# Optimization experiments

Measured on AMD Instinct MI355X. Metric: run time of the kernel, lower is better.

The kernel has to match this reference:

```python
import jax, jax.numpy as jnp
from jax import lax
import numpy as np

# Static module configuration (matches init_kwargs, idx=0)
B, T, H, W, C = 2, 8, 64, 64, 128
T_SP, H_SP, W_SP = 2, 64, 4          # idx=0 -> H_sp=resolution, W_sp=split_size
NUM_HEADS = 4
HEAD_DIM = C // NUM_HEADS
SCALE = HEAD_DIM ** -0.5
L = T * H * W
N = T_SP * H_SP * W_SP               # tokens per window = 512


def setup_inputs() -> dict:
    key = jax.random.key(0)
    k1, k2, k3 = jax.random.split(key, 3)
    return {
        "qkv": jax.random.normal(k1, (3, B, L, C), dtype=jnp.float32),
        "lepe_w": jax.random.normal(k2, (C, 1, 3, 3, 3), dtype=jnp.float32) * 0.05,  # depthwise Conv3d weight
        "lepe_b": jax.random.normal(k3, (C,), dtype=jnp.float32) * 0.05,
    }


def _to_windows(x):
    # x: (B, L, C) with L flattened as (T, H, W) -> (nW, N, C)
    x = x.reshape(B, T // T_SP, T_SP, H // H_SP, H_SP, W // W_SP, W_SP, C)
    x = x.transpose(0, 1, 3, 5, 2, 4, 6, 7)  # B, tB, hB, wB, T_sp, H_sp, W_sp, C
    return x.reshape(-1, N, C)


def reference(qkv, lepe_w, lepe_b):
    q, k, v = qkv[0], qkv[1], qkv[2]          # each (B, L, C)

    # q, k -> (nW, heads, N, head_dim)
    qw = _to_windows(q).reshape(-1, N, NUM_HEADS, HEAD_DIM).transpose(0, 2, 1, 3)
    kw = _to_windows(k).reshape(-1, N, NUM_HEADS, HEAD_DIM).transpose(0, 2, 1, 3)

    # v windows in NCDHW layout for the depthwise LePE conv: (nW, C, T_sp, H_sp, W_sp)
    v_sp = _to_windows(v).reshape(-1, T_SP, H_SP, W_SP, C).transpose(0, 4, 1, 2, 3)
    lepe = lax.conv_general_dilated(
        v_sp, lepe_w, window_strides=(1, 1, 1), padding='SAME',
        dimension_numbers=('NCDHW', 'OIDHW', 'NCDHW'), feature_group_count=C,
    ) + lepe_b[None, :, None, None, None]
    # match torch: reshape(-1, heads, head_dim, N).permute(0,1,3,2)
    lepe = lepe.reshape(-1, NUM_HEADS, HEAD_DIM, N).transpose(0, 1, 3, 2)
    vw = v_sp.reshape(-1, NUM_HEADS, HEAD_DIM, N).transpose(0, 1, 3, 2)

    # windowed attention (attn_drop = 0 in eval)
    attn = jax.nn.softmax(jnp.einsum('whnd,whmd->whnm', qw * SCALE, kw), axis=-1)
    out = jnp.einsum('whnm,whmd->whnd', attn, vw) + lepe     # (nW, heads, N, d)

    # merge heads and reverse window partition -> (B, L, C)
    out = out.transpose(0, 2, 1, 3).reshape(-1, N, C)
    out = out.reshape(B, T // T_SP, H // H_SP, W // W_SP, T_SP, H_SP, W_SP, C)
    out = out.transpose(0, 1, 4, 2, 5, 3, 6, 7).reshape(B, L, C)
    return out
```

## Files before the change

kernel.cpp:

```cpp
#include <hip/hip_runtime.h>
#include <hip/hip_fp16.h>

#define Bb 2
#define Tt 8
#define Hh 64
#define Ww 64
#define Cc 128
#define TSP 2
#define HSP 64
#define WSP 4
#define NH 4
#define HD 32
#define Ll (Tt*Hh*Ww)
#define Nn (TSP*HSP*WSP)
#define BLC (Bb*Ll*Cc)
#define QSCALE (0.17677669529663687f * 1.4426950408889634f)

typedef _Float16 half8_t __attribute__((ext_vector_type(8)));
typedef _Float16 half4_t __attribute__((ext_vector_type(4)));
typedef __fp16   fp16x4_t __attribute__((ext_vector_type(4)));
typedef __fp16   fp16x2_t __attribute__((ext_vector_type(2)));
typedef float   float4_t __attribute__((ext_vector_type(4)));

#if __has_builtin(__builtin_amdgcn_exp2f)
#define EXP2F(x) __builtin_amdgcn_exp2f(x)
#else
#define EXP2F(x) exp2f(x)
#endif

__device__ __forceinline__ int l_of(int tB, int xB, int n) {
    int ts = n >> 8;
    int ys = (n >> 2) & 63;
    int xs = n & 3;
    return tB*8192 + ts*4096 + ys*64 + xB*4 + xs;
}

__global__ __launch_bounds__(256, 4) void lepe_conv_kernel(
    const float* __restrict__ qkv, const float* __restrict__ wgt,
    const float* __restrict__ bias, float* __restrict__ out)
{
    __shared__ _Float16 vtok[Nn*HD];
    __shared__ _Float16 wl[27*HD];

    const int bid = blockIdx.x;
    const int w = bid >> 2, h = bid & 3;
    const int b = w >> 6, tB = (w >> 4) & 3, xB = w & 15;
    const int c0 = h*HD;
    const int t = threadIdx.x;

    const int j  = t & 7;
    const int nb = t >> 3;

    for (int r = 0; r < 16; ++r) {
        int n = r*32 + nb;
        int gi = (b*Ll + l_of(tB, xB, n))*Cc + c0 + j*4;
        float4_t f = *(const float4_t*)(qkv + 2*BLC + gi);
        half4_t hv;
        hv[0] = (_Float16)f.x; hv[1] = (_Float16)f.y;
        hv[2] = (_Float16)f.z; hv[3] = (_Float16)f.w;
        int cgp = j ^ (n & 7);
        *(half4_t*)(vtok + n*32 + cgp*4) = hv;
    }
    for (int i = t; i < 27*HD; i += 256) {
        int tap = i >> 5, d = i & 31;
        wl[i] = (_Float16)wgt[(c0 + d)*27 + tap];
    }
    __syncthreads();

    half4_t ww[27];
    #pragma unroll
    for (int tap = 0; tap < 27; ++tap)
        ww[tap] = *(const half4_t*)(wl + tap*32 + j*4);

    float4_t bi = *(const float4_t*)(bias + c0 + j*4);

    for (int r = 0; r < 16; ++r) {
        int n = r*32 + nb;
        int ts = n >> 8, ys = (n >> 2) & 63, xs = n & 3;
        half4_t acc = {(_Float16)0, (_Float16)0, (_Float16)0, (_Float16)0};
        #pragma unroll
        for (int dt = 0; dt < 3; ++dt) {
            int tt = ts + dt - 1;
            if ((unsigned)tt >= TSP) continue;
            #pragma unroll
            for (int dy = 0; dy < 3; ++dy) {
                int yy = ys + dy - 1;
                if ((unsigned)yy >= HSP) continue;
                #pragma unroll
                for (int dx = 0; dx < 3; ++dx) {
                    int xx = xs + dx - 1;
                    if ((unsigned)xx >= WSP) continue;
                    int nn = tt*256 + yy*4 + xx;
                    half4_t vv = *(const half4_t*)(vtok + nn*32 + ((j ^ (nn & 7)))*4);
                    acc += vv * ww[dt*9 + dy*3 + dx];
                }
            }
        }
        int gi = (b*Ll + l_of(tB, xB, n))*Cc + c0 + j*4;
        float4_t res;
        res.x = (float)acc[0] + bi.x; res.y = (float)acc[1] + bi.y;
        res.z = (float)acc[2] + bi.z; res.w = (float)acc[3] + bi.w;
        *(float4_t*)(out + gi) = res;
    }
}

__global__ __launch_bounds__(256, 2) void attn_kernel(
    const float* __restrict__ qkv, float* __restrict__ out)
{
    __shared__ _Float16 Ks[Nn*HD];
    __shared__ _Float16 Vt[HD*Nn];

    const int bid = blockIdx.x;
    const int w = bid >> 2, h = bid & 3;
    const int b = w >> 6, tB = (w >> 4) & 3, xB = w & 15;
    const int c0 = h*HD;
    const int t = threadIdx.x;
    const float* kg = qkv + BLC;
    const float* vg = qkv + 2*BLC;

    {
        const int j = t & 7, nb = t >> 3;
        for (int r = 0; r < 16; ++r) {
            int n = r*32 + nb;
            int gi = (b*Ll + l_of(tB, xB, n))*Cc + c0 + j*4;
            float4_t f = *(const float4_t*)(kg + gi);
            half4_t hv;
            hv[0] = (_Float16)f.x; hv[1] = (_Float16)f.y;
            hv[2] = (_Float16)f.z; hv[3] = (_Float16)f.w;
            *(half4_t*)(Ks + n*32 + j*4) = hv;
        }
    }
    {
        const int d = t & 31, chb = t >> 5;
        for (int r = 0; r < 16; ++r) {
            int ch = r*8 + chb;
            int n0 = ch*4;
            float f0 = vg[(b*Ll + l_of(tB, xB, n0+0))*Cc + c0 + d];
            float f1 = vg[(b*Ll + l_of(tB, xB, n0+1))*Cc + c0 + d];
            float f2 = vg[(b*Ll + l_of(tB, xB, n0+2))*Cc + c0 + d];
            float f3 = vg[(b*Ll + l_of(tB, xB, n0+3))*Cc + c0 + d];
            half4_t hv;
            hv[0] = (_Float16)f0; hv[1] = (_Float16)f1;
            hv[2] = (_Float16)f2; hv[3] = (_Float16)f3;
            *(half4_t*)(Vt + d*512 + (ch ^ (d & 15))*4) = hv;
        }
    }

    const int wv = t >> 6, lane = t & 63;
    const int c = lane & 15, quad = lane >> 4;
    const int qbase = wv*128;
    half8_t qf[8];
    #pragma unroll
    for (int nt = 0; nt < 8; ++nt) {
        int q = qbase + nt*16 + c;
        int gi = (b*Ll + l_of(tB, xB, q))*Cc + c0 + quad*8;
        float4_t f0 = *(const float4_t*)(qkv + gi);
        float4_t f1 = *(const float4_t*)(qkv + gi + 4);
        half8_t qv;
        qv[0] = (_Float16)(f0.x*QSCALE); qv[1] = (_Float16)(f0.y*QSCALE);
        qv[2] = (_Float16)(f0.z*QSCALE); qv[3] = (_Float16)(f0.w*QSCALE);
        qv[4] = (_Float16)(f1.x*QSCALE); qv[5] = (_Float16)(f1.y*QSCALE);
        qv[6] = (_Float16)(f1.z*QSCALE); qv[7] = (_Float16)(f1.w*QSCALE);
        qf[nt] = qv;
    }
    __syncthreads();

    float4_t acc[2][8];
    float4_t lacc[8];
    const float4_t fzero = {0.f, 0.f, 0.f, 0.f};
    const float4_t cshift = {-4.f, -4.f, -4.f, -4.f};
    #pragma unroll
    for (int nt = 0; nt < 8; ++nt) {
        lacc[nt] = fzero;
        acc[0][nt] = fzero; acc[1][nt] = fzero;
    }

    for (int kb = 0; kb < 16; ++kb) {
        const int k0 = kb*32;
        half8_t kf0 = *(const half8_t*)(Ks + (k0 +      c)*32 + quad*8);
        half8_t kf1 = *(const half8_t*)(Ks + (k0 + 16 + c)*32 + quad*8);

        fp16x4_t vf[2][2];
        #pragma unroll
        for (int mi = 0; mi < 2; ++mi) {
            #pragma unroll
            for (int ks = 0; ks < 2; ++ks) {
                int dim = mi*16 + c;
                int ch = kb*8 + ks*4 + quad;
                vf[mi][ks] = *(const fp16x4_t*)(Vt + dim*512 + (ch ^ c)*4);
            }
        }

        #pragma unroll
        for (int nt = 0; nt < 8; ++nt) {
            float4_t s0 = __builtin_amdgcn_mfma_f32_16x16x32_f16(kf0, qf[nt], cshift, 0, 0, 0);
            float4_t s1 = __builtin_amdgcn_mfma_f32_16x16x32_f16(kf1, qf[nt], cshift, 0, 0, 0);
            float4_t e0, e1;
            e0.x = EXP2F(s0.x); e0.y = EXP2F(s0.y);
            e0.z = EXP2F(s0.z); e0.w = EXP2F(s0.w);
            e1.x = EXP2F(s1.x); e1.y = EXP2F(s1.y);
            e1.z = EXP2F(s1.z); e1.w = EXP2F(s1.w);
            lacc[nt] += e0;
            lacc[nt] += e1;
            fp16x2_t a0 = __builtin_amdgcn_cvt_pkrtz(e0.x, e0.y);
            fp16x2_t a1 = __builtin_amdgcn_cvt_pkrtz(e0.z, e0.w);
            fp16x2_t b0 = __builtin_amdgcn_cvt_pkrtz(e1.x, e1.y);
            fp16x2_t b1 = __builtin_amdgcn_cvt_pkrtz(e1.z, e1.w);
            fp16x4_t ph0, ph1;
            ph0[0] = a0[0]; ph0[1] = a0[1]; ph0[2] = a1[0]; ph0[3] = a1[1];
            ph1[0] = b0[0]; ph1[1] = b0[1]; ph1[2] = b1[0]; ph1[3] = b1[1];
            acc[0][nt] = __builtin_amdgcn_mfma_f32_16x16x16f16(vf[0][0], ph0, acc[0][nt], 0, 0, 0);
            acc[0][nt] = __builtin_amdgcn_mfma_f32_16x16x16f16(vf[0][1], ph1, acc[0][nt], 0, 0, 0);
            acc[1][nt] = __builtin_amdgcn_mfma_f32_16x16x16f16(vf[1][0], ph0, acc[1][nt], 0, 0, 0);
            acc[1][nt] = __builtin_amdgcn_mfma_f32_16x16x16f16(vf[1][1], ph1, acc[1][nt], 0, 0, 0);
        }
    }

    #pragma unroll
    for (int nt = 0; nt < 8; ++nt) {
        float lpart = (lacc[nt].x + lacc[nt].y) + (lacc[nt].z + lacc[nt].w);
        lpart += __shfl_xor(lpart, 16, 64);
        lpart += __shfl_xor(lpart, 32, 64);
        float linv = 1.0f / lpart;
        int q = qbase + nt*16 + c;
        int gi = (b*Ll + l_of(tB, xB, q))*Cc + c0;
        #pragma unroll
        for (int mi = 0; mi < 2; ++mi) {
            float* p = out + gi + mi*16 + quad*4;
            float4_t prev = *(const float4_t*)p;
            float4_t r;
            r.x = acc[mi][nt].x*linv + prev.x;
            r.y = acc[mi][nt].y*linv + prev.y;
            r.z = acc[mi][nt].z*linv + prev.z;
            r.w = acc[mi][nt].w*linv + prev.w;
            *(float4_t*)p = r;
        }
    }
}

extern "C" void kernel_launch(void* const* d_in, const int* in_sizes, int n_in,
                              void* d_out, int out_size, void* d_ws, size_t ws_size,
                              hipStream_t stream) {
    const float* qkv  = (const float*)d_in[0];
    const float* wgt  = (const float*)d_in[1];
    const float* bias = (const float*)d_in[2];
    float* out = (float*)d_out;
    (void)d_ws; (void)ws_size; (void)in_sizes; (void)n_in; (void)out_size;

    hipLaunchKernelGGL(lepe_conv_kernel, dim3(512), dim3(256), 0, stream,
                       qkv, wgt, bias, out);
    hipLaunchKernelGGL(attn_kernel, dim3(512), dim3(256), 0, stream,
                       qkv, out);
}
```

Before: 195.3 us.

## Fuse LePE depthwise conv into attention kernel using transposed V in LDS

Removes the separate LePE conv kernel and computes the depthwise 3x3x3 conv inside the attention kernel from the already-staged transposed V tile, writing the result into the freed K shared buffer. The epilogue then adds LePE from LDS instead of read-modify-writing the output in global memory. This eliminates a second read of V, an output write plus re-read, and one launch. In exchange it adds extra LDS work, two block barriers and more register pressure in the attention kernel. It also simplifies V address computation using contiguous token strides.

```diff
diff --git a/kernel.cpp b/kernel.cpp
--- a/kernel.cpp
+++ b/kernel.cpp
@@ -28,6 +28,8 @@
 #define EXP2F(x) exp2f(x)
 #endif
 
+#define H4SPLAT(x) ((half4_t){(_Float16)(x), (_Float16)(x), (_Float16)(x), (_Float16)(x)})
+
 __device__ __forceinline__ int l_of(int tB, int xB, int n) {
     int ts = n >> 8;
     int ys = (n >> 2) & 63;
@@ -35,77 +37,9 @@
     return tB*8192 + ts*4096 + ys*64 + xB*4 + xs;
 }
 
-__global__ __launch_bounds__(256, 4) void lepe_conv_kernel(
+__global__ __launch_bounds__(256, 2) void fused_attn_kernel(
     const float* __restrict__ qkv, const float* __restrict__ wgt,
     const float* __restrict__ bias, float* __restrict__ out)
-{
-    __shared__ _Float16 vtok[Nn*HD];
-    __shared__ _Float16 wl[27*HD];
-
-    const int bid = blockIdx.x;
-    const int w = bid >> 2, h = bid & 3;
-    const int b = w >> 6, tB = (w >> 4) & 3, xB = w & 15;
-    const int c0 = h*HD;
-    const int t = threadIdx.x;
-
-    const int j  = t & 7;
-    const int nb = t >> 3;
-
-    for (int r = 0; r < 16; ++r) {
-        int n = r*32 + nb;
-        int gi = (b*Ll + l_of(tB, xB, n))*Cc + c0 + j*4;
-        float4_t f = *(const float4_t*)(qkv + 2*BLC + gi);
-        half4_t hv;
-        hv[0] = (_Float16)f.x; hv[1] = (_Float16)f.y;
-        hv[2] = (_Float16)f.z; hv[3] = (_Float16)f.w;
-        int cgp = j ^ (n & 7);
-        *(half4_t*)(vtok + n*32 + cgp*4) = hv;
-    }
-    for (int i = t; i < 27*HD; i += 256) {
-        int tap = i >> 5, d = i & 31;
-        wl[i] = (_Float16)wgt[(c0 + d)*27 + tap];
-    }
-    __syncthreads();
-
-    half4_t ww[27];
-    #pragma unroll
-    for (int tap = 0; tap < 27; ++tap)
-        ww[tap] = *(const half4_t*)(wl + tap*32 + j*4);
-
-    float4_t bi = *(const float4_t*)(bias + c0 + j*4);
-
-    for (int r = 0; r < 16; ++r) {
-        int n = r*32 + nb;
-        int ts = n >> 8, ys = (n >> 2) & 63, xs = n & 3;
-        half4_t acc = {(_Float16)0, (_Float16)0, (_Float16)0, (_Float16)0};
-        #pragma unroll
-        for (int dt = 0; dt < 3; ++dt) {
-            int tt = ts + dt - 1;
-            if ((unsigned)tt >= TSP) continue;
-            #pragma unroll
-            for (int dy = 0; dy < 3; ++dy) {
-                int yy = ys + dy - 1;
-                if ((unsigned)yy >= HSP) continue;
-                #pragma unroll
-                for (int dx = 0; dx < 3; ++dx) {
-                    int xx = xs + dx - 1;
-                    if ((unsigned)xx >= WSP) continue;
-                    int nn = tt*256 + yy*4 + xx;
-                    half4_t vv = *(const half4_t*)(vtok + nn*32 + ((j ^ (nn & 7)))*4);
-                    acc += vv * ww[dt*9 + dy*3 + dx];
-                }
-            }
-        }
-        int gi = (b*Ll + l_of(tB, xB, n))*Cc + c0 + j*4;
-        float4_t res;
-        res.x = (float)acc[0] + bi.x; res.y = (float)acc[1] + bi.y;
-        res.z = (float)acc[2] + bi.z; res.w = (float)acc[3] + bi.w;
-        *(float4_t*)(out + gi) = res;
-    }
-}
-
-__global__ __launch_bounds__(256, 2) void attn_kernel(
-    const float* __restrict__ qkv, float* __restrict__ out)
 {
     __shared__ _Float16 Ks[Nn*HD];
     __shared__ _Float16 Vt[HD*Nn];
@@ -135,10 +69,11 @@
         for (int r = 0; r < 16; ++r) {
             int ch = r*8 + chb;
             int n0 = ch*4;
-            float f0 = vg[(b*Ll + l_of(tB, xB, n0+0))*Cc + c0 + d];
-            float f1 = vg[(b*Ll + l_of(tB, xB, n0+1))*Cc + c0 + d];
-            float f2 = vg[(b*Ll + l_of(tB, xB, n0+2))*Cc + c0 + d];
-            float f3 = vg[(b*Ll + l_of(tB, xB, n0+3))*Cc + c0 + d];
+            int gi0 = (b*Ll + l_of(tB, xB, n0))*Cc + c0 + d;
+            float f0 = vg[gi0];
+            float f1 = vg[gi0 + Cc];
+            float f2 = vg[gi0 + 2*Cc];
+            float f3 = vg[gi0 + 3*Cc];
             half4_t hv;
             hv[0] = (_Float16)f0; hv[1] = (_Float16)f1;
             hv[2] = (_Float16)f2; hv[3] = (_Float16)f3;
@@ -216,6 +151,41 @@
         }
     }
 
+    __syncthreads();
+    {
+        const int d  = t & 31;
+        const int cb = t >> 5;
+        _Float16 wh[27];
+        #pragma unroll
+        for (int tap = 0; tap < 27; ++tap)
+            wh[tap] = (_Float16)wgt[(c0 + d)*27 + tap];
+        _Float16 bh = (_Float16)bias[c0 + d];
+
+        for (int i = 0; i < 16; ++i) {
+            int ch = cb*16 + i;
+            int ts = ch >> 6, ys = ch & 63;
+            half4_t acc4 = {bh, bh, bh, bh};
+            #pragma unroll
+            for (int dt = 0; dt < 3; ++dt) {
+                int tt = ts + dt - 1;
+                if ((unsigned)tt >= TSP) continue;
+                #pragma unroll
+                for (int dy = 0; dy < 3; ++dy) {
+                    int yy = ys + dy - 1;
+                    if ((unsigned)yy >= HSP) continue;
+                    int sc = tt*64 + yy;
+                    half4_t v4 = *(const half4_t*)(Vt + d*512 + (sc ^ (d & 15))*4);
+                    half4_t sm = {(_Float16)0, v4[0], v4[1], v4[2]};
+                    half4_t sp = {v4[1], v4[2], v4[3], (_Float16)0};
+                    const int tb = dt*9 + dy*3;
+                    acc4 += sm*H4SPLAT(wh[tb+0]) + v4*H4SPLAT(wh[tb+1]) + sp*H4SPLAT(wh[tb+2]);
+                }
+            }
+            *(half4_t*)(Ks + d*512 + (ch ^ (d & 15))*4) = acc4;
+        }
+    }
+    __syncthreads();
+
     #pragma unroll
     for (int nt = 0; nt < 8; ++nt) {
         float lpart = (lacc[nt].x + lacc[nt].y) + (lacc[nt].z + lacc[nt].w);
@@ -223,17 +193,18 @@
         lpart += __shfl_xor(lpart, 32, 64);
         float linv = 1.0f / lpart;
         int q = qbase + nt*16 + c;
+        int chq = q >> 2, eq = q & 3;
         int gi = (b*Ll + l_of(tB, xB, q))*Cc + c0;
         #pragma unroll
         for (int mi = 0; mi < 2; ++mi) {
-            float* p = out + gi + mi*16 + quad*4;
-            float4_t prev = *(const float4_t*)p;
             float4_t r;
-            r.x = acc[mi][nt].x*linv + prev.x;
-            r.y = acc[mi][nt].y*linv + prev.y;
-            r.z = acc[mi][nt].z*linv + prev.z;
-            r.w = acc[mi][nt].w*linv + prev.w;
-            *(float4_t*)p = r;
+            #pragma unroll
+            for (int rr = 0; rr < 4; ++rr) {
+                int dl = quad*4 + rr;
+                float lep = (float)Ks[(mi*16 + dl)*512 + (chq ^ dl)*4 + eq];
+                r[rr] = acc[mi][nt][rr]*linv + lep;
+            }
+            *(float4_t*)(out + gi + mi*16 + quad*4) = r;
         }
     }
 }
@@ -247,8 +218,6 @@
     float* out = (float*)d_out;
     (void)d_ws; (void)ws_size; (void)in_sizes; (void)n_in; (void)out_size;
 
-    hipLaunchKernelGGL(lepe_conv_kernel, dim3(512), dim3(256), 0, stream,
+    hipLaunchKernelGGL(fused_attn_kernel, dim3(512), dim3(256), 0, stream,
                        qkv, wgt, bias, out);
-    hipLaunchKernelGGL(attn_kernel, dim3(512), dim3(256), 0, stream,
-                       qkv, out);
 }
```

New measurement: 178.1 us. 1.1x faster.
